# Kernel optimization log

Hardware: AMD Instinct MI355X
Metric: run time of the kernel (lower is better)

## Reference

```python
import jax, jax.numpy as jnp
import numpy as np

N_NODES = 50000
N_EDGES = 800000
DIM = 128
N_LAYERS = 3  # IGNet gcnlayers default


def setup_inputs() -> dict:
    key = jax.random.key(0)
    k1, k2, k3 = jax.random.split(key, 3)
    h = jax.random.normal(k1, (N_NODES, DIM), dtype=jnp.float32)
    edge_src = jax.random.randint(k2, (N_EDGES,), 0, N_NODES, dtype=jnp.int32)
    edge_dst = jax.random.randint(k3, (N_EDGES,), 0, N_NODES, dtype=jnp.int32)
    return {"h": h, "edge_src": edge_src, "edge_dst": edge_dst}


def _sage_mean_layer(h, edge_src, edge_dst, deg):
    # DGL SAGEConv 'mean' with in_feats == out_feats in this repo:
    # lin_before_mp is False and the modified branch applies no linear,
    # so rst = h_self + mean_{u in N(v)} h_u  (0 for isolated nodes).
    msg = h[edge_src]                                   # [E, D] gather (copy_u)
    agg = jax.ops.segment_sum(msg, edge_dst, num_segments=h.shape[0])  # [N, D]
    neigh = agg / deg[:, None]
    return h + neigh


def reference(h, edge_src, edge_dst):
    n = h.shape[0]
    deg = jax.ops.segment_sum(
        jnp.ones((edge_dst.shape[0],), dtype=h.dtype), edge_dst, num_segments=n
    )
    deg = jnp.maximum(deg, 1.0)  # fn.mean yields 0 for zero-degree nodes
    # SAGENet.forward (eval: no DropEdge): outs = [h, l1/1, l2/2, l3/3]; res = sum(outs)
    res = h
    tmp = h
    for i in range(N_LAYERS):
        tmp = _sage_mean_layer(tmp, edge_src, edge_dst, deg)
        res = res + tmp / (1.0 + i)
    return res
```

## Files before the change

### kernel.cpp

```cpp
#include <hip/hip_runtime.h>

#define N_NODES 50000
#define N_EDGES 800000
#define SENTINEL 50000
#define SLOTS 64
#define NPX 6250
#define EP_GRID 2048

#ifndef __has_builtin
#define __has_builtin(x) 0
#endif
#if __has_builtin(__builtin_amdgcn_cvt_pk_f32_fp8) && __has_builtin(__builtin_amdgcn_cvt_pk_fp8_f32)
#define HWFP8 1
#else
#define HWFP8 0
#endif

typedef float vf2 __attribute__((ext_vector_type(2)));

__device__ __forceinline__ unsigned enc1_sw(float x) {
    unsigned u = __float_as_uint(x);
    unsigned s = (u >> 31) << 7;
    u &= 0x7fffffffu;
    if (u >= 0x43E00000u) return s | 0x7E;
    if (u < 0x3C800000u) {
        float m = __uint_as_float(u) * 512.0f;
        unsigned mi = (unsigned)__float2int_rn(m);
        return s | mi;
    }
    unsigned e = (u >> 23) - 120u;
    unsigned man = (u >> 20) & 7u;
    unsigned rest = u & 0xFFFFFu;
    if (rest > 0x80000u || (rest == 0x80000u && (man & 1u))) {
        man++;
        if (man == 8u) { man = 0u; e++; }
    }
    if (e > 15u || (e == 15u && man == 7u)) return s | 0x7E;
    return s | (e << 3) | man;
}
__device__ __forceinline__ float dec1_sw(unsigned b) {
    unsigned s = (b >> 7) & 1u, e = (b >> 3) & 15u, m = b & 7u;
    float v = e ? __uint_as_float(((e + 120u) << 23) | (m << 20))
                : (float)m * 0.001953125f;
    return s ? -v : v;
}
__device__ __forceinline__ unsigned enc4(float a, float b, float c, float d) {
#if HWFP8
    int w = __builtin_amdgcn_cvt_pk_fp8_f32(a, b, 0, false);
    w = __builtin_amdgcn_cvt_pk_fp8_f32(c, d, w, true);
    return (unsigned)w;
#else
    return enc1_sw(a) | (enc1_sw(b) << 8) | (enc1_sw(c) << 16) | (enc1_sw(d) << 24);
#endif
}

#if HWFP8
#define DEC8(w)                                                            \
    {                                                                      \
        vf2 p0 = __builtin_amdgcn_cvt_pk_f32_fp8((int)(w).x, false);       \
        vf2 p1 = __builtin_amdgcn_cvt_pk_f32_fp8((int)(w).x, true);        \
        vf2 p2 = __builtin_amdgcn_cvt_pk_f32_fp8((int)(w).y, false);       \
        vf2 p3 = __builtin_amdgcn_cvt_pk_f32_fp8((int)(w).y, true);        \
        a0 += p0[0]; a1 += p0[1]; a2 += p1[0]; a3 += p1[1];                \
        a4 += p2[0]; a5 += p2[1]; a6 += p3[0]; a7 += p3[1];                \
    }
#else
#define DEC8(w)                                                            \
    {                                                                      \
        a0 += dec1_sw((w).x & 0xffu);         a1 += dec1_sw(((w).x >> 8) & 0xffu); \
        a2 += dec1_sw(((w).x >> 16) & 0xffu); a3 += dec1_sw((w).x >> 24);  \
        a4 += dec1_sw((w).y & 0xffu);         a5 += dec1_sw(((w).y >> 8) & 0xffu); \
        a6 += dec1_sw(((w).y >> 16) & 0xffu); a7 += dec1_sw((w).y >> 24);  \
    }
#endif

__device__ __forceinline__ unsigned int pack_bf16x2(float x, float y) {
    unsigned int bx = __float_as_uint(x);
    unsigned int by = __float_as_uint(y);
    bx = (bx + 0x7fffu + ((bx >> 16) & 1u)) >> 16;
    by = (by + 0x7fffu + ((by >> 16) & 1u)) & 0xffff0000u;
    return (bx & 0xffffu) | by;
}
__device__ __forceinline__ float blo(unsigned int w) { return __uint_as_float(w << 16); }
__device__ __forceinline__ float bhi(unsigned int w) { return __uint_as_float(w & 0xffff0000u); }

__global__ void convert_kernel(const float* __restrict__ h,
                               unsigned* __restrict__ hf8,
                               unsigned* __restrict__ u1f8,
                               uint4* __restrict__ cursor4) {
    int idx = blockIdx.x * blockDim.x + threadIdx.x;
    if (idx < N_NODES / 4) cursor4[idx] = make_uint4(0, 0, 0, 0);
    if (idx >= (N_NODES + 1) * 32) return;
    if ((idx >> 5) == N_NODES) {
        hf8[idx] = 0u;
        u1f8[idx] = 0u;
    } else {
        float4 v = reinterpret_cast<const float4*>(h)[idx];
        hf8[idx] = enc4(v.x, v.y, v.z, v.w);
    }
}

__global__ void place_kernel(const int* __restrict__ edge_src,
                             const int* __restrict__ edge_dst,
                             int* __restrict__ cursor,
                             unsigned short* __restrict__ sorted_src) {
    int b = blockIdx.x;
    int lo = (b & 7) * NPX, hi = lo + NPX;
    for (int e = (b >> 3) * 256 + threadIdx.x; e < N_EDGES; e += 65536) {
        int d = edge_dst[e];
        if (d >= lo && d < hi) {
            int pos = atomicAdd(&cursor[d], 1);
            if (pos < SLOTS) sorted_src[(d << 6) + pos] = (unsigned short)edge_src[e];
        }
    }
}

template <bool FINAL>
__global__ void sage_layer_kernel(const unsigned short* __restrict__ sorted_src,
                                  const int* __restrict__ cursor,
                                  const uint2* __restrict__ srcf8,
                                  uint2* __restrict__ uf8_out,
                                  uint4* __restrict__ ubf_out,
                                  const float* __restrict__ h,
                                  const uint4* __restrict__ u1t,
                                  const uint4* __restrict__ u2t,
                                  float* __restrict__ res) {
    int gid = blockIdx.x * blockDim.x + threadIdx.x;
    int grp = gid >> 4;
    int sub = gid & 15;
    if (grp >= N_NODES) return;

    int degv = cursor[grp];
    int start = grp << 6;
    int dend = start + min(degv, SLOTS);

    float a0 = 0.f, a1 = 0.f, a2 = 0.f, a3 = 0.f;
    float a4 = 0.f, a5 = 0.f, a6 = 0.f, a7 = 0.f;

    for (int j = start; j < dend; j += 8) {
        uint4 ss = *reinterpret_cast<const uint4*>(sorted_src + j);
        unsigned i0 = ss.x & 0xffffu, i1 = ss.x >> 16;
        unsigned i2 = ss.y & 0xffffu, i3 = ss.y >> 16;
        unsigned i4 = ss.z & 0xffffu, i5 = ss.z >> 16;
        unsigned i6 = ss.w & 0xffffu, i7 = ss.w >> 16;
        if (j + 1 >= dend) i1 = SENTINEL;
        if (j + 2 >= dend) i2 = SENTINEL;
        if (j + 3 >= dend) i3 = SENTINEL;
        if (j + 4 >= dend) i4 = SENTINEL;
        if (j + 5 >= dend) i5 = SENTINEL;
        if (j + 6 >= dend) i6 = SENTINEL;
        if (j + 7 >= dend) i7 = SENTINEL;
        uint2 v0 = srcf8[i0 * 16 + sub];
        uint2 v1 = srcf8[i1 * 16 + sub];
        uint2 v2 = srcf8[i2 * 16 + sub];
        uint2 v3 = srcf8[i3 * 16 + sub];
        uint2 v4 = srcf8[i4 * 16 + sub];
        uint2 v5 = srcf8[i5 * 16 + sub];
        uint2 v6 = srcf8[i6 * 16 + sub];
        uint2 v7 = srcf8[i7 * 16 + sub];
        DEC8(v0) DEC8(v1) DEC8(v2) DEC8(v3)
        DEC8(v4) DEC8(v5) DEC8(v6) DEC8(v7)
    }

    float inv = 1.0f / (float)max(degv, 1);
    a0 *= inv; a1 *= inv; a2 *= inv; a3 *= inv;
    a4 *= inv; a5 *= inv; a6 *= inv; a7 *= inv;

    if (!FINAL) {
        uint2 w8;
        w8.x = enc4(a0, a1, a2, a3);
        w8.y = enc4(a4, a5, a6, a7);
        uf8_out[grp * 16 + sub] = w8;
        uint4 b;
        b.x = pack_bf16x2(a0, a1);
        b.y = pack_bf16x2(a2, a3);
        b.z = pack_bf16x2(a4, a5);
        b.w = pack_bf16x2(a6, a7);
        ubf_out[grp * 16 + sub] = b;
    } else {
        const float C0 = 2.8333333f, C1 = 3.0f, C2 = 1.5f, C3 = 0.33333334f;
        uint4 w1 = u1t[grp * 16 + sub];
        uint4 w2 = u2t[grp * 16 + sub];
        const float4* h4 = reinterpret_cast<const float4*>(h);
        float4* res4 = reinterpret_cast<float4*>(res);
        int fb = grp * 32 + sub * 2;
        float4 h0 = h4[fb], h1 = h4[fb + 1];
        float4 r0, r1;
        r0.x = C0 * h0.x + C1 * blo(w1.x) + C2 * blo(w2.x) + C3 * a0;
        r0.y = C0 * h0.y + C1 * bhi(w1.x) + C2 * bhi(w2.x) + C3 * a1;
        r0.z = C0 * h0.z + C1 * blo(w1.y) + C2 * blo(w2.y) + C3 * a2;
        r0.w = C0 * h0.w + C1 * bhi(w1.y) + C2 * bhi(w2.y) + C3 * a3;
        r1.x = C0 * h1.x + C1 * blo(w1.z) + C2 * blo(w2.z) + C3 * a4;
        r1.y = C0 * h1.y + C1 * bhi(w1.z) + C2 * bhi(w2.z) + C3 * a5;
        r1.z = C0 * h1.z + C1 * blo(w1.w) + C2 * blo(w2.w) + C3 * a6;
        r1.w = C0 * h1.w + C1 * bhi(w1.w) + C2 * bhi(w2.w) + C3 * a7;
        res4[fb] = r0;
        res4[fb + 1] = r1;
    }
}

extern "C" void kernel_launch(void* const* d_in, const int* in_sizes, int n_in,
                              void* d_out, int out_size, void* d_ws, size_t ws_size,
                              hipStream_t stream) {
    const float* h        = (const float*)d_in[0];
    const int*   edge_src = (const int*)d_in[1];
    const int*   edge_dst = (const int*)d_in[2];
    float*       res      = (float*)d_out;

    char* ws = (char*)d_ws;
    int* cursor            = (int*)(ws + 0x000000);
    unsigned short* sorted = (unsigned short*)(ws + 0x040000);
    unsigned* hf8          = (unsigned*)(ws + 0x700000);
    unsigned* u1f8         = (unsigned*)(ws + 0xE00000);
    unsigned* u1b          = (unsigned*)(ws + 0x1500000);
    unsigned* u2b          = (unsigned*)(ws + 0x2200000);
    unsigned* u2f8         = hf8;

    const int BLK = 256;

    convert_kernel<<<((N_NODES + 1) * 32 + BLK - 1) / BLK, BLK, 0, stream>>>(
        h, hf8, u1f8, (uint4*)cursor);

    place_kernel<<<EP_GRID, BLK, 0, stream>>>(edge_src, edge_dst, cursor, sorted);

    const int LGRID = (N_NODES * 16 + BLK - 1) / BLK;
    sage_layer_kernel<false><<<LGRID, BLK, 0, stream>>>(
        sorted, cursor, (const uint2*)hf8, (uint2*)u1f8, (uint4*)u1b,
        nullptr, nullptr, nullptr, nullptr);
    sage_layer_kernel<false><<<LGRID, BLK, 0, stream>>>(
        sorted, cursor, (const uint2*)u1f8, (uint2*)u2f8, (uint4*)u2b,
        nullptr, nullptr, nullptr, nullptr);
    sage_layer_kernel<true><<<LGRID, BLK, 0, stream>>>(
        sorted, cursor, (const uint2*)u2f8, nullptr, nullptr,
        h, (const uint4*)u1b, (const uint4*)u2b, res);
}
```

Measured before the change: 110.3 us.

## Split each SAGE layer into two feature-half passes to shrink gather working set

Each layer's gather-aggregate kernel is split into two launches, each covering half of the 128 feature columns with 8 threads per node instead of 16. Each pass gathers only 64 bytes per source node, so the randomly accessed source table it touches is half the size and more likely to stay resident in L2/MALL. The cost is reading the sorted index lists and cursors twice per layer and three extra kernel launches.

```diff
diff --git a/kernel.cpp b/kernel.cpp
--- a/kernel.cpp
+++ b/kernel.cpp
@@ -116,23 +116,25 @@
 }
 
 template <bool FINAL>
-__global__ void sage_layer_kernel(const unsigned short* __restrict__ sorted_src,
-                                  const int* __restrict__ cursor,
-                                  const uint2* __restrict__ srcf8,
-                                  uint2* __restrict__ uf8_out,
-                                  uint4* __restrict__ ubf_out,
-                                  const float* __restrict__ h,
-                                  const uint4* __restrict__ u1t,
-                                  const uint4* __restrict__ u2t,
-                                  float* __restrict__ res) {
+__global__ void sage_half_kernel(const unsigned short* __restrict__ sorted_src,
+                                 const int* __restrict__ cursor,
+                                 const uint2* __restrict__ srcf8,
+                                 uint2* __restrict__ uf8_out,
+                                 uint4* __restrict__ ubf_out,
+                                 const float* __restrict__ h,
+                                 const uint4* __restrict__ u1t,
+                                 const uint4* __restrict__ u2t,
+                                 float* __restrict__ res,
+                                 int half) {
     int gid = blockIdx.x * blockDim.x + threadIdx.x;
-    int grp = gid >> 4;
-    int sub = gid & 15;
+    int grp = gid >> 3;
+    int sub = gid & 7;
     if (grp >= N_NODES) return;
 
     int degv = cursor[grp];
     int start = grp << 6;
     int dend = start + min(degv, SLOTS);
+    int off = half * 8 + sub;
 
     float a0 = 0.f, a1 = 0.f, a2 = 0.f, a3 = 0.f;
     float a4 = 0.f, a5 = 0.f, a6 = 0.f, a7 = 0.f;
@@ -150,14 +152,14 @@
         if (j + 5 >= dend) i5 = SENTINEL;
         if (j + 6 >= dend) i6 = SENTINEL;
         if (j + 7 >= dend) i7 = SENTINEL;
-        uint2 v0 = srcf8[i0 * 16 + sub];
-        uint2 v1 = srcf8[i1 * 16 + sub];
-        uint2 v2 = srcf8[i2 * 16 + sub];
-        uint2 v3 = srcf8[i3 * 16 + sub];
-        uint2 v4 = srcf8[i4 * 16 + sub];
-        uint2 v5 = srcf8[i5 * 16 + sub];
-        uint2 v6 = srcf8[i6 * 16 + sub];
-        uint2 v7 = srcf8[i7 * 16 + sub];
+        uint2 v0 = srcf8[i0 * 16 + off];
+        uint2 v1 = srcf8[i1 * 16 + off];
+        uint2 v2 = srcf8[i2 * 16 + off];
+        uint2 v3 = srcf8[i3 * 16 + off];
+        uint2 v4 = srcf8[i4 * 16 + off];
+        uint2 v5 = srcf8[i5 * 16 + off];
+        uint2 v6 = srcf8[i6 * 16 + off];
+        uint2 v7 = srcf8[i7 * 16 + off];
         DEC8(v0) DEC8(v1) DEC8(v2) DEC8(v3)
         DEC8(v4) DEC8(v5) DEC8(v6) DEC8(v7)
     }
@@ -170,20 +172,20 @@
         uint2 w8;
         w8.x = enc4(a0, a1, a2, a3);
         w8.y = enc4(a4, a5, a6, a7);
-        uf8_out[grp * 16 + sub] = w8;
+        uf8_out[grp * 16 + off] = w8;
         uint4 b;
         b.x = pack_bf16x2(a0, a1);
         b.y = pack_bf16x2(a2, a3);
         b.z = pack_bf16x2(a4, a5);
         b.w = pack_bf16x2(a6, a7);
-        ubf_out[grp * 16 + sub] = b;
+        ubf_out[grp * 16 + off] = b;
     } else {
         const float C0 = 2.8333333f, C1 = 3.0f, C2 = 1.5f, C3 = 0.33333334f;
-        uint4 w1 = u1t[grp * 16 + sub];
-        uint4 w2 = u2t[grp * 16 + sub];
+        uint4 w1 = u1t[grp * 16 + off];
+        uint4 w2 = u2t[grp * 16 + off];
         const float4* h4 = reinterpret_cast<const float4*>(h);
         float4* res4 = reinterpret_cast<float4*>(res);
-        int fb = grp * 32 + sub * 2;
+        int fb = grp * 32 + half * 16 + sub * 2;
         float4 h0 = h4[fb], h1 = h4[fb + 1];
         float4 r0, r1;
         r0.x = C0 * h0.x + C1 * blo(w1.x) + C2 * blo(w2.x) + C3 * a0;
@@ -223,14 +225,23 @@
 
     place_kernel<<<EP_GRID, BLK, 0, stream>>>(edge_src, edge_dst, cursor, sorted);
 
-    const int LGRID = (N_NODES * 16 + BLK - 1) / BLK;
-    sage_layer_kernel<false><<<LGRID, BLK, 0, stream>>>(
+    const int HGRID = (N_NODES * 8 + BLK - 1) / BLK;
+    sage_half_kernel<false><<<HGRID, BLK, 0, stream>>>(
         sorted, cursor, (const uint2*)hf8, (uint2*)u1f8, (uint4*)u1b,
-        nullptr, nullptr, nullptr, nullptr);
-    sage_layer_kernel<false><<<LGRID, BLK, 0, stream>>>(
+        nullptr, nullptr, nullptr, nullptr, 0);
+    sage_half_kernel<false><<<HGRID, BLK, 0, stream>>>(
+        sorted, cursor, (const uint2*)hf8, (uint2*)u1f8, (uint4*)u1b,
+        nullptr, nullptr, nullptr, nullptr, 1);
+    sage_half_kernel<false><<<HGRID, BLK, 0, stream>>>(
         sorted, cursor, (const uint2*)u1f8, (uint2*)u2f8, (uint4*)u2b,
-        nullptr, nullptr, nullptr, nullptr);
-    sage_layer_kernel<true><<<LGRID, BLK, 0, stream>>>(
+        nullptr, nullptr, nullptr, nullptr, 0);
+    sage_half_kernel<false><<<HGRID, BLK, 0, stream>>>(
+        sorted, cursor, (const uint2*)u1f8, (uint2*)u2f8, (uint4*)u2b,
+        nullptr, nullptr, nullptr, nullptr, 1);
+    sage_half_kernel<true><<<HGRID, BLK, 0, stream>>>(
         sorted, cursor, (const uint2*)u2f8, nullptr, nullptr,
-        h, (const uint4*)u1b, (const uint4*)u2b, res);
-}
+        h, (const uint4*)u1b, (const uint4*)u2b, res, 0);
+    sage_half_kernel<true><<<HGRID, BLK, 0, stream>>>(
+        sorted, cursor, (const uint2*)u2f8, nullptr, nullptr,
+        h, (const uint4*)u1b, (const uint4*)u2b, res, 1);
+}
```

Result: slower. 140.3 us (+27.1%).

## Replace global-atomic edge placement with two-pass partition and shared-memory bucketing

Applied to the files above, without the earlier changes.

Replaces the single place kernel, which did a global atomicAdd per edge on node cursors, with two passes. First, a partition kernel splits edges into 8 destination ranges per sub-stream, using block-local counters and packed (src,dst) records. Second, a bucket kernel builds each 250-node range's slot table in shared memory and writes it out with coalesced stores. This trades global atomic contention and scattered 2-byte writes for an extra pass over an intermediate stream buffer. The stream buffer reuses the u2b workspace region, which is only written later by layer 2.

```diff
diff --git a/kernel.cpp b/kernel.cpp
--- a/kernel.cpp
+++ b/kernel.cpp
@@ -5,7 +5,12 @@
 #define SENTINEL 50000
 #define SLOTS 64
 #define NPX 6250
-#define EP_GRID 2048
+#define NSUB 32
+#define CAP_SUB 4096
+#define PART_BLOCKS 800
+#define EPB 1000
+#define RANGE 250
+#define BUCKET_BLOCKS 200
 
 #ifndef __has_builtin
 #define __has_builtin(x) 0
@@ -87,9 +92,9 @@
 __global__ void convert_kernel(const float* __restrict__ h,
                                unsigned* __restrict__ hf8,
                                unsigned* __restrict__ u1f8,
-                               uint4* __restrict__ cursor4) {
+                               int* __restrict__ gcnt) {
     int idx = blockIdx.x * blockDim.x + threadIdx.x;
-    if (idx < N_NODES / 4) cursor4[idx] = make_uint4(0, 0, 0, 0);
+    if (idx < 8 * NSUB * 16) gcnt[idx] = 0;
     if (idx >= (N_NODES + 1) * 32) return;
     if ((idx >> 5) == N_NODES) {
         hf8[idx] = 0u;
@@ -100,19 +105,61 @@
     }
 }
 
-__global__ void place_kernel(const int* __restrict__ edge_src,
-                             const int* __restrict__ edge_dst,
-                             int* __restrict__ cursor,
-                             unsigned short* __restrict__ sorted_src) {
-    int b = blockIdx.x;
-    int lo = (b & 7) * NPX, hi = lo + NPX;
-    for (int e = (b >> 3) * 256 + threadIdx.x; e < N_EDGES; e += 65536) {
-        int d = edge_dst[e];
-        if (d >= lo && d < hi) {
-            int pos = atomicAdd(&cursor[d], 1);
-            if (pos < SLOTS) sorted_src[(d << 6) + pos] = (unsigned short)edge_src[e];
+__global__ void partition_kernel(const int* __restrict__ edge_src,
+                                 const int* __restrict__ edge_dst,
+                                 int* __restrict__ gcnt,
+                                 unsigned* __restrict__ streams) {
+    __shared__ int cnt[8], base[8], cnt2[8];
+    int b = blockIdx.x, t = threadIdx.x;
+    int sub = b & (NSUB - 1);
+    if (t < 8) { cnt[t] = 0; cnt2[t] = 0; }
+    __syncthreads();
+    int e0 = b * EPB;
+    for (int i = t; i < EPB; i += 256) {
+        int d = edge_dst[e0 + i];
+        atomicAdd(&cnt[d / NPX], 1);
+    }
+    __syncthreads();
+    if (t < 8) base[t] = atomicAdd(&gcnt[(t * NSUB + sub) * 16], cnt[t]);
+    __syncthreads();
+    for (int i = t; i < EPB; i += 256) {
+        int d = edge_dst[e0 + i];
+        int s = edge_src[e0 + i];
+        int x = d / NPX;
+        int off = atomicAdd(&cnt2[x], 1);
+        streams[(x * NSUB + sub) * CAP_SUB + base[x] + off] =
+            (unsigned)s | ((unsigned)d << 16);
+    }
+}
+
+__global__ void bucket_kernel(const unsigned* __restrict__ streams,
+                              const int* __restrict__ gcnt,
+                              int* __restrict__ cursor,
+                              unsigned short* __restrict__ sorted_src) {
+    __shared__ int cur[RANGE];
+    __shared__ unsigned short stage[RANGE * SLOTS];
+    int b = blockIdx.x, t = threadIdx.x;
+    int s = b & 7;
+    int n0 = s * NPX + (b >> 3) * RANGE;
+    for (int i = t; i < RANGE; i += 256) cur[i] = 0;
+    __syncthreads();
+    for (int sub = 0; sub < NSUB; ++sub) {
+        int cnt = gcnt[(s * NSUB + sub) * 16];
+        const unsigned* st = streams + (s * NSUB + sub) * CAP_SUB;
+        for (int i = t; i < cnt; i += 256) {
+            unsigned rec = st[i];
+            int dl = (int)(rec >> 16) - n0;
+            if ((unsigned)dl < RANGE) {
+                int pos = atomicAdd(&cur[dl], 1);
+                if (pos < SLOTS) stage[dl * SLOTS + pos] = (unsigned short)(rec & 0xffffu);
+            }
         }
     }
+    __syncthreads();
+    const uint4* st4 = reinterpret_cast<const uint4*>(stage);
+    uint4* out4 = reinterpret_cast<uint4*>(sorted_src + n0 * SLOTS);
+    for (int i = t; i < RANGE * SLOTS / 8; i += 256) out4[i] = st4[i];
+    for (int i = t; i < RANGE; i += 256) cursor[n0 + i] = cur[i];
 }
 
 template <bool FINAL>
@@ -209,19 +256,22 @@
 
     char* ws = (char*)d_ws;
     int* cursor            = (int*)(ws + 0x000000);
-    unsigned short* sorted = (unsigned short*)(ws + 0x040000);
+    int* gcnt              = (int*)(ws + 0x040000);
+    unsigned short* sorted = (unsigned short*)(ws + 0x050000);
     unsigned* hf8          = (unsigned*)(ws + 0x700000);
     unsigned* u1f8         = (unsigned*)(ws + 0xE00000);
     unsigned* u1b          = (unsigned*)(ws + 0x1500000);
     unsigned* u2b          = (unsigned*)(ws + 0x2200000);
+    unsigned* streams      = (unsigned*)(ws + 0x2200000);
     unsigned* u2f8         = hf8;
 
     const int BLK = 256;
 
     convert_kernel<<<((N_NODES + 1) * 32 + BLK - 1) / BLK, BLK, 0, stream>>>(
-        h, hf8, u1f8, (uint4*)cursor);
-
-    place_kernel<<<EP_GRID, BLK, 0, stream>>>(edge_src, edge_dst, cursor, sorted);
+        h, hf8, u1f8, gcnt);
+
+    partition_kernel<<<PART_BLOCKS, BLK, 0, stream>>>(edge_src, edge_dst, gcnt, streams);
+    bucket_kernel<<<BUCKET_BLOCKS, BLK, 0, stream>>>(streams, gcnt, cursor, sorted);
 
     const int LGRID = (N_NODES * 16 + BLK - 1) / BLK;
     sage_layer_kernel<false><<<LGRID, BLK, 0, stream>>>(
```

New measurement: 196.1 us. 77.7% more time.

## Replace atomic scatter placement with two-pass bucketed partition and shared-memory sort

Applied to the files above, without the earlier changes.

Replaces the single edge placement kernel, which did a global atomic per edge into per-node cursors across 8 range-filtered passes, with a two-stage scheme. A partition kernel bins edges into 64-node buckets, sharded 8 ways, using packed records. A bucket kernel then builds each bucket's slot lists in shared memory with shared atomics and writes them out as coalesced uint4 stores. This removes most scattered global atomics and 2-byte writes, at the cost of an extra launch and a temporary buffer that reuses the u2b region. Sub-buckets are capped at 256 entries, so skewed degree distributions could drop edges.

```diff
diff --git a/kernel.cpp b/kernel.cpp
--- a/kernel.cpp
+++ b/kernel.cpp
@@ -4,8 +4,9 @@
 #define N_EDGES 800000
 #define SENTINEL 50000
 #define SLOTS 64
-#define NPX 6250
-#define EP_GRID 2048
+#define NBKT 782
+#define NSH 8
+#define CAP_SUB 256
 
 #ifndef __has_builtin
 #define __has_builtin(x) 0
@@ -87,9 +88,9 @@
 __global__ void convert_kernel(const float* __restrict__ h,
                                unsigned* __restrict__ hf8,
                                unsigned* __restrict__ u1f8,
-                               uint4* __restrict__ cursor4) {
+                               int* __restrict__ gcnt) {
     int idx = blockIdx.x * blockDim.x + threadIdx.x;
-    if (idx < N_NODES / 4) cursor4[idx] = make_uint4(0, 0, 0, 0);
+    if (idx < NSH * NBKT) gcnt[idx] = 0;
     if (idx >= (N_NODES + 1) * 32) return;
     if ((idx >> 5) == N_NODES) {
         hf8[idx] = 0u;
@@ -100,19 +101,50 @@
     }
 }
 
-__global__ void place_kernel(const int* __restrict__ edge_src,
-                             const int* __restrict__ edge_dst,
-                             int* __restrict__ cursor,
-                             unsigned short* __restrict__ sorted_src) {
-    int b = blockIdx.x;
-    int lo = (b & 7) * NPX, hi = lo + NPX;
-    for (int e = (b >> 3) * 256 + threadIdx.x; e < N_EDGES; e += 65536) {
-        int d = edge_dst[e];
-        if (d >= lo && d < hi) {
-            int pos = atomicAdd(&cursor[d], 1);
-            if (pos < SLOTS) sorted_src[(d << 6) + pos] = (unsigned short)edge_src[e];
+__global__ void partition_kernel(const int* __restrict__ edge_src,
+                                 const int* __restrict__ edge_dst,
+                                 int* __restrict__ gcnt,
+                                 unsigned* __restrict__ streams) {
+    int e = blockIdx.x * 256 + threadIdx.x;
+    if (e >= N_EDGES) return;
+    int sh = blockIdx.x & 7;
+    int d = edge_dst[e];
+    int s = edge_src[e];
+    int b = d >> 6;
+    int pos = atomicAdd(&gcnt[sh * NBKT + b], 1);
+    if (pos < CAP_SUB)
+        streams[(sh * NBKT + b) * CAP_SUB + pos] =
+            (unsigned)s | ((unsigned)(d & 63) << 16);
+}
+
+__global__ void bucket_kernel(const unsigned* __restrict__ streams,
+                              const int* __restrict__ gcnt,
+                              int* __restrict__ cursor,
+                              unsigned short* __restrict__ sorted_src) {
+    __shared__ int cur[64];
+    __shared__ unsigned short stage[64 * SLOTS];
+    int b = blockIdx.x, t = threadIdx.x;
+    int n0 = b << 6;
+    int nn = min(64, N_NODES - n0);
+    if (t < 64) cur[t] = 0;
+    __syncthreads();
+#pragma unroll
+    for (int sh = 0; sh < NSH; ++sh) {
+        int cnt = min(gcnt[sh * NBKT + b], CAP_SUB);
+        const unsigned* st = streams + (sh * NBKT + b) * CAP_SUB;
+        for (int i = t; i < cnt; i += 256) {
+            unsigned rec = st[i];
+            int dl = rec >> 16;
+            int pos = atomicAdd(&cur[dl], 1);
+            if (pos < SLOTS) stage[dl * SLOTS + pos] = (unsigned short)(rec & 0xffffu);
         }
     }
+    __syncthreads();
+    const uint4* st4 = reinterpret_cast<const uint4*>(stage);
+    uint4* out4 = reinterpret_cast<uint4*>(sorted_src + (size_t)n0 * SLOTS);
+    int n4 = nn * SLOTS / 8;
+    for (int i = t; i < n4; i += 256) out4[i] = st4[i];
+    if (t < nn) cursor[n0 + t] = cur[t];
 }
 
 template <bool FINAL>
@@ -208,20 +240,24 @@
     float*       res      = (float*)d_out;
 
     char* ws = (char*)d_ws;
-    int* cursor            = (int*)(ws + 0x000000);
-    unsigned short* sorted = (unsigned short*)(ws + 0x040000);
+    int* gcnt              = (int*)(ws + 0x000000);
+    int* cursor            = (int*)(ws + 0x010000);
+    unsigned short* sorted = (unsigned short*)(ws + 0x050000);
     unsigned* hf8          = (unsigned*)(ws + 0x700000);
     unsigned* u1f8         = (unsigned*)(ws + 0xE00000);
     unsigned* u1b          = (unsigned*)(ws + 0x1500000);
     unsigned* u2b          = (unsigned*)(ws + 0x2200000);
+    unsigned* streams      = (unsigned*)(ws + 0x2200000);
     unsigned* u2f8         = hf8;
 
     const int BLK = 256;
 
     convert_kernel<<<((N_NODES + 1) * 32 + BLK - 1) / BLK, BLK, 0, stream>>>(
-        h, hf8, u1f8, (uint4*)cursor);
-
-    place_kernel<<<EP_GRID, BLK, 0, stream>>>(edge_src, edge_dst, cursor, sorted);
+        h, hf8, u1f8, gcnt);
+
+    partition_kernel<<<(N_EDGES + BLK - 1) / BLK, BLK, 0, stream>>>(
+        edge_src, edge_dst, gcnt, streams);
+    bucket_kernel<<<NBKT, BLK, 0, stream>>>(streams, gcnt, cursor, sorted);
 
     const int LGRID = (N_NODES * 16 + BLK - 1) / BLK;
     sage_layer_kernel<false><<<LGRID, BLK, 0, stream>>>(
```

Measured after the change: 127.8 us. +15.8%, slower.
